# Performance work log

Measured on AMD Instinct MI355X. Metric: run time of the kernel, lower is better.

Reference implementation:

```python
import jax, jax.numpy as jnp
import numpy as np


def setup_inputs() -> dict:
    key = jax.random.key(0)
    kq, kk, kv = jax.random.split(key, 3)
    B, S, D = 4, 4096, 64
    Q = jax.random.normal(kq, (B, S, D), dtype=jnp.float32)
    K = jax.random.normal(kk, (B, S, D), dtype=jnp.float32)
    V = jax.random.normal(kv, (B, S, D), dtype=jnp.float32)
    return {"Q": Q, "K": K, "V": V}


def reference(Q, K, V):
    # nom = Q @ K^T  -> [B, Sq, Sk]
    # Original code does K.transpose_(1,2) in place BEFORE reading K.shape[1],
    # so demon = sqrt(d_head) (standard scaling).
    d = K.shape[-1]
    scores = jnp.einsum('bqd,bkd->bqk', Q, K) / jnp.sqrt(jnp.float32(d))
    # Faithful quirk: nn.Softmax(dim=1) normalizes over the QUERY axis (axis=1).
    attn = jax.nn.softmax(scores, axis=1)
    return jnp.einsum('bqk,bkd->bqd', attn, V)
```

## Files before the change

### kernel.cpp

```cpp
#include <hip/hip_runtime.h>


#define B_N 4
#define S_N 4096
#define D_N 64
#define BS_N (B_N * S_N)
#define NCHUNK 128
#define IMG_CH16 4096
#define QSC (0.125f * 1.44269504088896f)

typedef __attribute__((ext_vector_type(4))) float f32x4;
typedef __attribute__((ext_vector_type(2))) float f32x2;
typedef __attribute__((ext_vector_type(8))) _Float16 half8;
typedef unsigned char uchar;

#define MFMAH(A, Bf, C) __builtin_amdgcn_mfma_f32_16x16x32_f16((A), (Bf), (C), 0, 0, 0)

__device__ __forceinline__ void gld16(const void* g, void* l) {
  __builtin_amdgcn_global_load_lds((const __attribute__((address_space(1))) unsigned int*)g,
                                   (__attribute__((address_space(3))) unsigned int*)l, 16, 0, 0);
}

__global__ __launch_bounds__(256) void sdpa_prepKQ19(const float* __restrict__ K,
                                                     const float* __restrict__ Qm,
                                                     uchar* __restrict__ K16,
                                                     uchar* __restrict__ Q16) {
  const int sel = blockIdx.x >> 9;
  const int c = blockIdx.x & 127;
  const int b = (blockIdx.x >> 7) & 3;
  const int t = threadIdx.x;
  const int r = t >> 3;
  const int d0 = (t & 7) * 8;
  const float* src = (sel ? Qm : K) + ((size_t)(b * S_N + c * 32 + r)) * D_N + d0;
  f32x4 x0 = *(const f32x4*)(src);
  f32x4 x1 = *(const f32x4*)(src + 4);
  const float scale = sel ? QSC : 1.0f;
  x0 *= scale; x1 *= scale;
  half8 hf;
#pragma unroll
  for (int j = 0; j < 4; ++j) { hf[j] = (_Float16)x0[j]; hf[4 + j] = (_Float16)x1[j]; }
  const int kt = r >> 4;
  const int lane = ((d0 & 31) >> 3) * 16 + (r & 15);
  uchar* img = sel ? Q16 : K16;
  *(half8*)(img + ((size_t)(b * NCHUNK + c)) * IMG_CH16 + kt * 2048 + (d0 >> 5) * 1024 + lane * 16) = hf;
}

__global__ __launch_bounds__(256, 4) void sdpa_stats16(const uchar* __restrict__ K16,
                                                       const uchar* __restrict__ Q16,
                                                       float* __restrict__ lPart) {
  const int tid = threadIdx.x, lane = tid & 63, w = tid >> 6;
  const int l15 = lane & 15, g4 = lane >> 4;
  const int xcd = blockIdx.x & 7;
  const int b = xcd >> 1;
  const int r = blockIdx.x >> 3;
  const int kt = ((r & 31) << 1) | (xcd & 1);
  const int qs = ((r >> 5) << 2) | w;

  half8 kf[4][2];
#pragma unroll
  for (int kg = 0; kg < 4; ++kg) {
    const uchar* kc = K16 + ((size_t)(b * NCHUNK + kt * 2 + (kg >> 1))) * IMG_CH16
                    + (kg & 1) * 2048 + lane * 16;
    kf[kg][0] = *(const half8*)(kc);
    kf[kg][1] = *(const half8*)(kc + 1024);
  }

  float lacc[4][4];
#pragma unroll
  for (int kg = 0; kg < 4; ++kg)
#pragma unroll
    for (int rr = 0; rr < 4; ++rr) lacc[kg][rr] = 0.f;

  const uchar* Qbase = Q16 + ((size_t)(b * NCHUNK + qs * 8)) * IMG_CH16 + lane * 16;

#pragma unroll 1
  for (int it = 0; it < 8; ++it) {
    const uchar* Qc = Qbase + (size_t)it * IMG_CH16;
#pragma unroll
    for (int qt = 0; qt < 2; ++qt) {
      half8 qf0 = *(const half8*)(Qc + qt * 2048);
      half8 qf1 = *(const half8*)(Qc + qt * 2048 + 1024);
#pragma unroll
      for (int kg = 0; kg < 4; ++kg) {
        f32x4 acc = {0.f, 0.f, 0.f, 0.f};
        acc = MFMAH(kf[kg][0], qf0, acc);
        acc = MFMAH(kf[kg][1], qf1, acc);
#pragma unroll
        for (int rr = 0; rr < 4; ++rr)
          lacc[kg][rr] += exp2f(acc[rr]);
      }
    }
  }

#pragma unroll
  for (int off = 1; off < 16; off <<= 1)
#pragma unroll
    for (int kg = 0; kg < 4; ++kg)
#pragma unroll
      for (int rr = 0; rr < 4; ++rr)
        lacc[kg][rr] += __shfl_xor(lacc[kg][rr], off);

  if (l15 == 0) {
#pragma unroll
    for (int kg = 0; kg < 4; ++kg)
#pragma unroll
      for (int rr = 0; rr < 4; ++rr)
        lPart[(size_t)qs * BS_N + b * S_N + kt * 64 + kg * 16 + (g4 << 2) + rr] = lacc[kg][rr];
  }
}

__global__ __launch_bounds__(256) void sdpa_prepV8(const float* __restrict__ V,
                                                   const float* __restrict__ lPart,
                                                   uchar* __restrict__ VT) {
  __shared__ float Vs[32][65];
  __shared__ float rls[32];
  const int c = blockIdx.x & 127;
  const int b = blockIdx.x >> 7;
  const int t = threadIdx.x;
  {
    const int k = t >> 3;
    const int d0 = (t & 7) * 8;
    const float* src = V + ((size_t)(b * S_N + c * 32 + k)) * D_N + d0;
    f32x4 x0 = *(const f32x4*)(src);
    f32x4 x1 = *(const f32x4*)(src + 4);
#pragma unroll
    for (int j = 0; j < 4; ++j) { Vs[k][d0 + j] = x0[j]; Vs[k][d0 + 4 + j] = x1[j]; }
    if (t < 32) {
      float s = 0.f;
      const float* lp = lPart + b * S_N + c * 32 + t;
#pragma unroll
      for (int j = 0; j < 16; ++j) s += lp[(size_t)j * BS_N];
      rls[t] = 1.0f / s;
    }
  }
  __syncthreads();
  const int d = t >> 2;
  const int kg = t & 3;
  half8 hf;
#pragma unroll
  for (int j = 0; j < 8; ++j) {
    const int cc = kg * 8 + j;
    const int k = (((cc >> 2) & 1) << 4) + (((cc >> 3)) << 2) + (cc & 3);
    hf[j] = (_Float16)(Vs[k][d] * rls[k]);
  }
  const int lane = kg * 16 + (d & 15);
  *(half8*)(VT + ((size_t)(b * NCHUNK + c)) * IMG_CH16 + (d >> 4) * 1024 + lane * 16) = hf;
}

__global__ __launch_bounds__(1024, 4) void sdpa_apply19(const float* __restrict__ Q,
                                                        const uchar* __restrict__ K16,
                                                        const uchar* __restrict__ VTimg,
                                                        float* __restrict__ Out) {
  __shared__ __attribute__((aligned(16))) uchar sm[131072];

  const int tid = threadIdx.x, lane = tid & 63, w = tid >> 6;
  const int l15 = lane & 15, g4 = lane >> 4;
  const int qsub = w >> 3, kq = w & 7;
  const int xcd = blockIdx.x & 7;
  const int b = xcd >> 1;
  const int qt = ((blockIdx.x >> 3) << 1) | (xcd & 1);

  half8 qf[2][2];
#pragma unroll
  for (int qg = 0; qg < 2; ++qg) {
    const int qRow = qt * 64 + qsub * 32 + qg * 16 + l15;
    const float* Qp = Q + ((size_t)(b * S_N + qRow)) * D_N;
    f32x4 x0 = *(const f32x4*)(Qp + g4 * 8);
    f32x4 x1 = *(const f32x4*)(Qp + g4 * 8 + 4);
    f32x4 y0 = *(const f32x4*)(Qp + 32 + g4 * 8);
    f32x4 y1 = *(const f32x4*)(Qp + 36 + g4 * 8);
    x0 *= QSC; x1 *= QSC; y0 *= QSC; y1 *= QSC;
#pragma unroll
    for (int j = 0; j < 4; ++j) {
      qf[qg][0][j] = (_Float16)x0[j]; qf[qg][0][4 + j] = (_Float16)x1[j];
      qf[qg][1][j] = (_Float16)y0[j]; qf[qg][1][4 + j] = (_Float16)y1[j];
    }
  }

  f32x4 accO[2][4];
#pragma unroll
  for (int qg = 0; qg < 2; ++qg)
#pragma unroll
    for (int dt = 0; dt < 4; ++dt) accO[qg][dt] = (f32x4){0.f, 0.f, 0.f, 0.f};

  const uchar* Kc = K16 + ((size_t)(b * NCHUNK + kq * 16)) * IMG_CH16 + lane * 16;
  const uchar* Vc = VTimg + ((size_t)(b * NCHUNK + kq * 16)) * IMG_CH16 + lane * 16;
  uchar* const slab = sm + kq * 16384;
  const int l16 = lane * 16;

#define STAGE(IT, PAR)                                                         \
  {                                                                            \
    uchar* dst = slab + (PAR) * 8192 + (qsub == 0 ? 4096 : 0);                 \
    const uchar* src = (qsub == 0 ? Vc : Kc) + (size_t)(IT) * IMG_CH16;        \
    _Pragma("unroll")                                                          \
    for (int s = 0; s < 4; ++s) gld16(src + s * 1024, dst + s * 1024);         \
  }

  STAGE(0, 0)
  asm volatile("s_waitcnt vmcnt(0)" ::: "memory");
  __syncthreads();

#pragma unroll 1
  for (int it = 0; it < 16; ++it) {
    const int par = it & 1;
    if (it < 15) STAGE(it + 1, par ^ 1)
    __builtin_amdgcn_sched_barrier(0);

    const uchar* ks = slab + par * 8192;
    const uchar* vs = ks + 4096;

    half8 paF[2];
#pragma unroll
    for (int kt = 0; kt < 2; ++kt) {
      half8 kf0 = *(const half8*)(ks + kt * 2048 + l16);
      half8 kf1 = *(const half8*)(ks + kt * 2048 + 1024 + l16);
#pragma unroll
      for (int qg = 0; qg < 2; ++qg) {
        f32x4 acc = {0.f, 0.f, 0.f, 0.f};
        acc = MFMAH(kf0, qf[qg][0], acc);
        acc = MFMAH(kf1, qf[qg][1], acc);
#pragma unroll
        for (int rr = 0; rr < 4; ++rr)
          paF[qg][kt * 4 + rr] = (_Float16)exp2f(acc[rr]);
      }
    }

#pragma unroll
    for (int dt = 0; dt < 4; ++dt) {
      half8 vf = *(const half8*)(vs + dt * 1024 + l16);
#pragma unroll
      for (int qg = 0; qg < 2; ++qg)
        accO[qg][dt] = MFMAH(paF[qg], vf, accO[qg][dt]);
    }

    asm volatile("s_waitcnt vmcnt(0)" ::: "memory");
    __syncthreads();
  }

#undef STAGE

  float* Comb = (float*)sm;
#pragma unroll
  for (int qg = 0; qg < 2; ++qg) {
    __syncthreads();
    {
      float* CombW = Comb + w * (16 * 68);
#pragma unroll
      for (int dt = 0; dt < 4; ++dt)
#pragma unroll
        for (int r = 0; r < 4; ++r)
          CombW[((g4 << 2) + r) * 68 + dt * 16 + l15] = accO[qg][dt][r];
    }
    __syncthreads();
    {
      const int qs2 = tid >> 9;
      const int row = (tid >> 5) & 15;
      const int c2 = (tid & 31) * 2;
      f32x2 s = {0.f, 0.f};
#pragma unroll
      for (int kq2 = 0; kq2 < 8; ++kq2)
        s += *(const f32x2*)(Comb + (qs2 * 8 + kq2) * (16 * 68) + row * 68 + c2);
      *(f32x2*)(Out + ((size_t)(b * S_N + qt * 64 + qs2 * 32 + qg * 16 + row)) * D_N + c2) = s;
    }
  }
}

extern "C" void kernel_launch(void* const* d_in, const int* in_sizes, int n_in,
                              void* d_out, int out_size, void* d_ws, size_t ws_size,
                              hipStream_t stream) {
  (void)in_sizes; (void)n_in; (void)out_size;
  const float* Q = (const float*)d_in[0];
  const float* K = (const float*)d_in[1];
  const float* V = (const float*)d_in[2];
  float* out = (float*)d_out;
  uchar* ws = (uchar*)d_ws;

  const size_t img16 = (size_t)B_N * NCHUNK * IMG_CH16;
  const size_t offK16 = 0;
  const size_t offQ16 = img16;
  const size_t offLP = 2 * img16;
  const size_t need = offLP + (size_t)16 * BS_N * 4;

  if (ws_size < need) return;
  float* lPart = (float*)(ws + offLP);

  sdpa_prepKQ19<<<dim3(1024), dim3(256), 0, stream>>>(K, Q, ws + offK16, ws + offQ16);
  sdpa_stats16<<<dim3(1024), dim3(256), 0, stream>>>(ws + offK16, ws + offQ16, lPart);
  sdpa_prepV8<<<dim3(512), dim3(256), 0, stream>>>(V, lPart, ws + offQ16);
  sdpa_apply19<<<dim3(256), dim3(1024), 0, stream>>>(Q, ws + offK16, ws + offQ16, out);
}
```

Measured before the change: 61.46 us.

## Split apply kernel key range across two blocks with atomic output accumulation

The apply kernel now splits each block's key range in half across two blocks (kh) and doubles the queries per block. Each block keeps four k-chunk wave groups instead of eight, which cuts shared memory from 128KB to 68KB and may allow higher occupancy. Partial outputs from the two halves are combined with float atomicAdd into an output zeroed by a memset. The change adds a memset launch and atomic traffic, and makes the summation order nondeterministic.

```diff
diff --git a/kernel.cpp b/kernel.cpp
--- a/kernel.cpp
+++ b/kernel.cpp
@@ -147,23 +147,26 @@
   *(half8*)(VT + ((size_t)(b * NCHUNK + c)) * IMG_CH16 + (d >> 4) * 1024 + lane * 16) = hf;
 }
 
-__global__ __launch_bounds__(1024, 4) void sdpa_apply19(const float* __restrict__ Q,
+__global__ __launch_bounds__(1024, 4) void sdpa_apply20(const float* __restrict__ Q,
                                                         const uchar* __restrict__ K16,
                                                         const uchar* __restrict__ VTimg,
                                                         float* __restrict__ Out) {
-  __shared__ __attribute__((aligned(16))) uchar sm[131072];
+  __shared__ __attribute__((aligned(16))) uchar sm[69632];
 
   const int tid = threadIdx.x, lane = tid & 63, w = tid >> 6;
   const int l15 = lane & 15, g4 = lane >> 4;
-  const int qsub = w >> 3, kq = w & 7;
+  const int qsub = w >> 2, kq = w & 3;
   const int xcd = blockIdx.x & 7;
   const int b = xcd >> 1;
-  const int qt = ((blockIdx.x >> 3) << 1) | (xcd & 1);
+  const int qlow = xcd & 1;
+  const int rest = blockIdx.x >> 3;
+  const int kh = rest & 1;
+  const int qt = ((rest >> 1) << 1) | qlow;
 
   half8 qf[2][2];
 #pragma unroll
   for (int qg = 0; qg < 2; ++qg) {
-    const int qRow = qt * 64 + qsub * 32 + qg * 16 + l15;
+    const int qRow = qt * 128 + qsub * 32 + qg * 16 + l15;
     const float* Qp = Q + ((size_t)(b * S_N + qRow)) * D_N;
     f32x4 x0 = *(const f32x4*)(Qp + g4 * 8);
     f32x4 x1 = *(const f32x4*)(Qp + g4 * 8 + 4);
@@ -183,17 +186,20 @@
 #pragma unroll
     for (int dt = 0; dt < 4; ++dt) accO[qg][dt] = (f32x4){0.f, 0.f, 0.f, 0.f};
 
-  const uchar* Kc = K16 + ((size_t)(b * NCHUNK + kq * 16)) * IMG_CH16 + lane * 16;
-  const uchar* Vc = VTimg + ((size_t)(b * NCHUNK + kq * 16)) * IMG_CH16 + lane * 16;
+  const uchar* Kc = K16 + ((size_t)(b * NCHUNK + kh * 64 + kq * 16)) * IMG_CH16 + lane * 16;
+  const uchar* Vc = VTimg + ((size_t)(b * NCHUNK + kh * 64 + kq * 16)) * IMG_CH16 + lane * 16;
   uchar* const slab = sm + kq * 16384;
   const int l16 = lane * 16;
 
 #define STAGE(IT, PAR)                                                         \
   {                                                                            \
-    uchar* dst = slab + (PAR) * 8192 + (qsub == 0 ? 4096 : 0);                 \
-    const uchar* src = (qsub == 0 ? Vc : Kc) + (size_t)(IT) * IMG_CH16;        \
+    uchar* dstB = slab + (PAR) * 8192;                                         \
     _Pragma("unroll")                                                          \
-    for (int s = 0; s < 4; ++s) gld16(src + s * 1024, dst + s * 1024);         \
+    for (int si = 0; si < 2; ++si) {                                           \
+      const int s = qsub * 2 + si;                                             \
+      const uchar* src = (s < 4 ? Kc : Vc) + (size_t)(IT) * IMG_CH16 + (s & 3) * 1024; \
+      gld16(src, dstB + s * 1024);                                             \
+    }                                                                          \
   }
 
   STAGE(0, 0)
@@ -253,14 +259,19 @@
     }
     __syncthreads();
     {
-      const int qs2 = tid >> 9;
-      const int row = (tid >> 5) & 15;
-      const int c2 = (tid & 31) * 2;
-      f32x2 s = {0.f, 0.f};
-#pragma unroll
-      for (int kq2 = 0; kq2 < 8; ++kq2)
-        s += *(const f32x2*)(Comb + (qs2 * 8 + kq2) * (16 * 68) + row * 68 + c2);
-      *(f32x2*)(Out + ((size_t)(b * S_N + qt * 64 + qs2 * 32 + qg * 16 + row)) * D_N + c2) = s;
+      const int qs2 = tid >> 8;
+      const int row = (tid >> 4) & 15;
+      const int c4 = (tid & 15) * 4;
+      f32x4 s = {0.f, 0.f, 0.f, 0.f};
+#pragma unroll
+      for (int kq2 = 0; kq2 < 4; ++kq2)
+        s += *(const f32x4*)(Comb + (qs2 * 4 + kq2) * (16 * 68) + row * 68 + c4);
+      const int q = qt * 128 + qs2 * 32 + qg * 16 + row;
+      float* op = Out + ((size_t)(b * S_N + q)) * D_N + c4;
+      atomicAdd(op + 0, s[0]);
+      atomicAdd(op + 1, s[1]);
+      atomicAdd(op + 2, s[2]);
+      atomicAdd(op + 3, s[3]);
     }
   }
 }
@@ -268,7 +279,7 @@
 extern "C" void kernel_launch(void* const* d_in, const int* in_sizes, int n_in,
                               void* d_out, int out_size, void* d_ws, size_t ws_size,
                               hipStream_t stream) {
-  (void)in_sizes; (void)n_in; (void)out_size;
+  (void)in_sizes; (void)n_in;
   const float* Q = (const float*)d_in[0];
   const float* K = (const float*)d_in[1];
   const float* V = (const float*)d_in[2];
@@ -284,8 +295,9 @@
   if (ws_size < need) return;
   float* lPart = (float*)(ws + offLP);
 
+  hipMemsetAsync(out, 0, (size_t)out_size * sizeof(float), stream);
   sdpa_prepKQ19<<<dim3(1024), dim3(256), 0, stream>>>(K, Q, ws + offK16, ws + offQ16);
   sdpa_stats16<<<dim3(1024), dim3(256), 0, stream>>>(ws + offK16, ws + offQ16, lPart);
   sdpa_prepV8<<<dim3(512), dim3(256), 0, stream>>>(V, lPart, ws + offQ16);
-  sdpa_apply19<<<dim3(256), dim3(1024), 0, stream>>>(Q, ws + offK16, ws + offQ16, out);
-}
+  sdpa_apply20<<<dim3(256), dim3(1024), 0, stream>>>(Q, ws + offK16, ws + offQ16, out);
+}
```

Result: slower. 92.03 us (+49.7%).

## Fuse K/Q fp16 conversion into stats kernel and drop prep launch

Applied to the files above, without the earlier changes.

Removes the separate K/Q conversion kernel. The stats kernel now reads fp32 K and Q directly, converting and scaling them to fp16 in registers, and the qs==0 blocks also write the packed K16 image that the apply kernel needs. This saves one kernel launch and the write-then-read round trip of the Q16 image. In exchange, each stats block re-reads fp32 Q (twice the bytes of fp16) across all K tiles and repeats the conversion arithmetic, so total memory traffic inside the stats kernel goes up.

```diff
diff --git a/kernel.cpp b/kernel.cpp
--- a/kernel.cpp
+++ b/kernel.cpp
@@ -21,33 +21,17 @@
                                    (__attribute__((address_space(3))) unsigned int*)l, 16, 0, 0);
 }
 
-__global__ __launch_bounds__(256) void sdpa_prepKQ19(const float* __restrict__ K,
-                                                     const float* __restrict__ Qm,
-                                                     uchar* __restrict__ K16,
-                                                     uchar* __restrict__ Q16) {
-  const int sel = blockIdx.x >> 9;
-  const int c = blockIdx.x & 127;
-  const int b = (blockIdx.x >> 7) & 3;
-  const int t = threadIdx.x;
-  const int r = t >> 3;
-  const int d0 = (t & 7) * 8;
-  const float* src = (sel ? Qm : K) + ((size_t)(b * S_N + c * 32 + r)) * D_N + d0;
-  f32x4 x0 = *(const f32x4*)(src);
-  f32x4 x1 = *(const f32x4*)(src + 4);
-  const float scale = sel ? QSC : 1.0f;
-  x0 *= scale; x1 *= scale;
-  half8 hf;
-#pragma unroll
-  for (int j = 0; j < 4; ++j) { hf[j] = (_Float16)x0[j]; hf[4 + j] = (_Float16)x1[j]; }
-  const int kt = r >> 4;
-  const int lane = ((d0 & 31) >> 3) * 16 + (r & 15);
-  uchar* img = sel ? Q16 : K16;
-  *(half8*)(img + ((size_t)(b * NCHUNK + c)) * IMG_CH16 + kt * 2048 + (d0 >> 5) * 1024 + lane * 16) = hf;
-}
-
-__global__ __launch_bounds__(256, 4) void sdpa_stats16(const uchar* __restrict__ K16,
-                                                       const uchar* __restrict__ Q16,
-                                                       float* __restrict__ lPart) {
+__device__ __forceinline__ half8 cvt8(const f32x4 a, const f32x4 b) {
+  half8 h;
+#pragma unroll
+  for (int j = 0; j < 4; ++j) { h[j] = (_Float16)a[j]; h[4 + j] = (_Float16)b[j]; }
+  return h;
+}
+
+__global__ __launch_bounds__(256, 4) void sdpa_stats16c(const float* __restrict__ K,
+                                                        const float* __restrict__ Qm,
+                                                        uchar* __restrict__ K16,
+                                                        float* __restrict__ lPart) {
   const int tid = threadIdx.x, lane = tid & 63, w = tid >> 6;
   const int l15 = lane & 15, g4 = lane >> 4;
   const int xcd = blockIdx.x & 7;
@@ -59,10 +43,24 @@
   half8 kf[4][2];
 #pragma unroll
   for (int kg = 0; kg < 4; ++kg) {
-    const uchar* kc = K16 + ((size_t)(b * NCHUNK + kt * 2 + (kg >> 1))) * IMG_CH16
-                    + (kg & 1) * 2048 + lane * 16;
-    kf[kg][0] = *(const half8*)(kc);
-    kf[kg][1] = *(const half8*)(kc + 1024);
+    const int row = kt * 64 + kg * 16 + l15;
+    const float* Kp = K + ((size_t)(b * S_N + row)) * D_N;
+    f32x4 a0 = *(const f32x4*)(Kp + g4 * 8);
+    f32x4 a1 = *(const f32x4*)(Kp + g4 * 8 + 4);
+    f32x4 b0 = *(const f32x4*)(Kp + 32 + g4 * 8);
+    f32x4 b1 = *(const f32x4*)(Kp + 36 + g4 * 8);
+    kf[kg][0] = cvt8(a0, a1);
+    kf[kg][1] = cvt8(b0, b1);
+  }
+
+  if (qs == 0) {
+#pragma unroll
+    for (int kg = 0; kg < 4; ++kg) {
+      uchar* base = K16 + ((size_t)(b * NCHUNK + kt * 2 + (kg >> 1))) * IMG_CH16
+                  + (kg & 1) * 2048 + lane * 16;
+      *(half8*)(base) = kf[kg][0];
+      *(half8*)(base + 1024) = kf[kg][1];
+    }
   }
 
   float lacc[4][4];
@@ -71,15 +69,20 @@
 #pragma unroll
     for (int rr = 0; rr < 4; ++rr) lacc[kg][rr] = 0.f;
 
-  const uchar* Qbase = Q16 + ((size_t)(b * NCHUNK + qs * 8)) * IMG_CH16 + lane * 16;
+  const float* Qb = Qm + ((size_t)(b * S_N + qs * 256)) * D_N;
 
 #pragma unroll 1
   for (int it = 0; it < 8; ++it) {
-    const uchar* Qc = Qbase + (size_t)it * IMG_CH16;
 #pragma unroll
     for (int qt = 0; qt < 2; ++qt) {
-      half8 qf0 = *(const half8*)(Qc + qt * 2048);
-      half8 qf1 = *(const half8*)(Qc + qt * 2048 + 1024);
+      const float* Qp = Qb + ((size_t)(it * 32 + qt * 16 + l15)) * D_N;
+      f32x4 a0 = *(const f32x4*)(Qp + g4 * 8);
+      f32x4 a1 = *(const f32x4*)(Qp + g4 * 8 + 4);
+      f32x4 b0 = *(const f32x4*)(Qp + 32 + g4 * 8);
+      f32x4 b1 = *(const f32x4*)(Qp + 36 + g4 * 8);
+      a0 *= QSC; a1 *= QSC; b0 *= QSC; b1 *= QSC;
+      half8 qf0 = cvt8(a0, a1);
+      half8 qf1 = cvt8(b0, b1);
 #pragma unroll
       for (int kg = 0; kg < 4; ++kg) {
         f32x4 acc = {0.f, 0.f, 0.f, 0.f};
@@ -170,11 +173,8 @@
     f32x4 y0 = *(const f32x4*)(Qp + 32 + g4 * 8);
     f32x4 y1 = *(const f32x4*)(Qp + 36 + g4 * 8);
     x0 *= QSC; x1 *= QSC; y0 *= QSC; y1 *= QSC;
-#pragma unroll
-    for (int j = 0; j < 4; ++j) {
-      qf[qg][0][j] = (_Float16)x0[j]; qf[qg][0][4 + j] = (_Float16)x1[j];
-      qf[qg][1][j] = (_Float16)y0[j]; qf[qg][1][4 + j] = (_Float16)y1[j];
-    }
+    qf[qg][0] = cvt8(x0, x1);
+    qf[qg][1] = cvt8(y0, y1);
   }
 
   f32x4 accO[2][4];
@@ -277,15 +277,14 @@
 
   const size_t img16 = (size_t)B_N * NCHUNK * IMG_CH16;
   const size_t offK16 = 0;
-  const size_t offQ16 = img16;
+  const size_t offVT = img16;
   const size_t offLP = 2 * img16;
   const size_t need = offLP + (size_t)16 * BS_N * 4;
 
   if (ws_size < need) return;
   float* lPart = (float*)(ws + offLP);
 
-  sdpa_prepKQ19<<<dim3(1024), dim3(256), 0, stream>>>(K, Q, ws + offK16, ws + offQ16);
-  sdpa_stats16<<<dim3(1024), dim3(256), 0, stream>>>(ws + offK16, ws + offQ16, lPart);
-  sdpa_prepV8<<<dim3(512), dim3(256), 0, stream>>>(V, lPart, ws + offQ16);
-  sdpa_apply19<<<dim3(256), dim3(1024), 0, stream>>>(Q, ws + offK16, ws + offQ16, out);
-}
+  sdpa_stats16c<<<dim3(1024), dim3(256), 0, stream>>>(K, Q, ws + offK16, lPart);
+  sdpa_prepV8<<<dim3(512), dim3(256), 0, stream>>>(V, lPart, ws + offVT);
+  sdpa_apply19<<<dim3(256), dim3(1024), 0, stream>>>(Q, ws + offK16, ws + offVT, out);
+}
```

Measured after the change: 76.11 us. +23.8%, slower.
